# Kernel tuning notes

Hardware: AMD Instinct MI355X
Metric: run time of the kernel (lower is better)

The kernel has to match this reference:

```python
import jax, jax.numpy as jnp
import numpy as np
import math

B, T, N, E = 16, 12, 2000, 8000
D, GAT_HEADS, NHEAD, FF, L, HORIZON = 64, 4, 4, 128, 2, 3
M = B * N  # batched node count


def setup_inputs() -> dict:
    key = jax.random.key(0)
    ks = jax.random.split(key, 16)

    def nrm(k, shape, s=0.1):
        return jax.random.normal(k, shape, jnp.float32) * s

    return dict(
        x_seq=jax.random.normal(ks[0], (B, T, N), jnp.float32),
        edge_index=jax.random.randint(ks[1], (2, E), 0, N),
        # GATConv 1: in_dim=1 -> 4 heads x 8 = 32
        W1=nrm(ks[2], (1, 32)),
        att_src1=nrm(ks[3], (GAT_HEADS, 8)),
        att_dst1=nrm(ks[4], (GAT_HEADS, 8)),
        b1=jnp.zeros((32,), jnp.float32),
        # GATConv 2: 32 -> 4 heads x 16 = 64
        W2=nrm(ks[5], (32, 64)),
        att_src2=nrm(ks[6], (GAT_HEADS, 16)),
        att_dst2=nrm(ks[7], (GAT_HEADS, 16)),
        b2=jnp.zeros((64,), jnp.float32),
        # TransformerEncoder (post-LN, relu), stacked over L layers
        Wqkv=nrm(ks[8], (L, 3 * D, D)), bqkv=jnp.zeros((L, 3 * D), jnp.float32),
        Wo=nrm(ks[9], (L, D, D)), bo=jnp.zeros((L, D), jnp.float32),
        Wf1=nrm(ks[10], (L, FF, D)), bf1=jnp.zeros((L, FF), jnp.float32),
        Wf2=nrm(ks[11], (L, D, FF)), bf2=jnp.zeros((L, D), jnp.float32),
        g1=jnp.ones((L, D), jnp.float32), be1=jnp.zeros((L, D), jnp.float32),
        g2=jnp.ones((L, D), jnp.float32), be2=jnp.zeros((L, D), jnp.float32),
        # prediction head
        Wh=nrm(ks[12], (HORIZON, D)), bh=jnp.zeros((HORIZON,), jnp.float32),
    )


def _layer_norm(x, g, b, eps=1e-5):
    mu = x.mean(-1, keepdims=True)
    var = ((x - mu) ** 2).mean(-1, keepdims=True)
    return (x - mu) * jax.lax.rsqrt(var + eps) * g + b


def _gat(x, src, dst, W, a_src, a_dst, bias, H, C, num_nodes):
    # PyG GATConv (concat=True, eval mode). x: [M, in] -> [M, H*C]
    h = (x @ W).reshape(-1, H, C)                                  # [M,H,C]
    e = jax.nn.leaky_relu((h * a_src).sum(-1)[src] + (h * a_dst).sum(-1)[dst], 0.2)  # [Etot,H]
    m = jax.ops.segment_max(e, dst, num_segments=num_nodes)
    w = jnp.exp(e - m[dst])
    s = jax.ops.segment_sum(w, dst, num_segments=num_nodes)
    alpha = w / (s[dst] + 1e-16)
    out = jax.ops.segment_sum(h[src] * alpha[:, :, None], dst, num_segments=num_nodes)
    return out.reshape(-1, H * C) + bias


def _forward(x_seq, edge_index, W1, att_src1, att_dst1, b1, W2, att_src2, att_dst2, b2,
             Wqkv, bqkv, Wo, bo, Wf1, bf1, Wf2, bf2, g1, be1, g2, be2, Wh, bh):
    # batch edge index with per-graph node offsets, then add self loops (PyG default)
    offs = (jnp.arange(B) * N)[:, None]
    loops = jnp.arange(M)
    src = jnp.concatenate([(edge_index[0][None] + offs).reshape(-1), loops])
    dst = jnp.concatenate([(edge_index[1][None] + offs).reshape(-1), loops])

    xt = x_seq.transpose(1, 0, 2).reshape(T, M, 1)  # per-timestep node features

    def gnn_step(x):
        h = jax.nn.relu(_gat(x, src, dst, W1, att_src1, att_dst1, b1, GAT_HEADS, 8, M))
        return jax.nn.relu(_gat(h, src, dst, W2, att_src2, att_dst2, b2, GAT_HEADS, 16, M))

    seq = jax.vmap(gnn_step)(xt)  # [T, M, D]

    # sinusoidal positional encoding over time axis
    pos = jnp.arange(T, dtype=jnp.float32)[:, None]
    div = jnp.exp(jnp.arange(0, D, 2, dtype=jnp.float32) * (-math.log(10000.0) / D))
    pe = jnp.zeros((T, D), jnp.float32)
    pe = pe.at[:, 0::2].set(jnp.sin(pos * div)).at[:, 1::2].set(jnp.cos(pos * div))
    seq = seq + pe[:, None, :]

    hd = D // NHEAD
    scale = 1.0 / math.sqrt(hd)
    for i in range(L):  # post-LN transformer encoder layers
        qkv = seq @ Wqkv[i].T + bqkv[i]
        q, k, v = jnp.split(qkv, 3, axis=-1)
        q = q.reshape(T, M, NHEAD, hd)
        k = k.reshape(T, M, NHEAD, hd)
        v = v.reshape(T, M, NHEAD, hd)
        sc = jnp.einsum('tmhd,smhd->mhts', q, k) * scale  # [M,H,T,T]
        attn = jax.nn.softmax(sc, axis=-1)
        o = jnp.einsum('mhts,smhd->tmhd', attn, v).reshape(T, M, D)
        seq = _layer_norm(seq + (o @ Wo[i].T + bo[i]), g1[i], be1[i])
        ff = jax.nn.relu(seq @ Wf1[i].T + bf1[i]) @ Wf2[i].T + bf2[i]
        seq = _layer_norm(seq + ff, g2[i], be2[i])

    final = seq[-1]  # [M, D]
    return (final @ Wh.T + bh).reshape(B, N, HORIZON).transpose(0, 2, 1)  # [B, horizon, N]


def reference(x_seq, edge_index, W1, att_src1, att_dst1, b1, W2, att_src2, att_dst2, b2,
              Wqkv, bqkv, Wo, bo, Wf1, bf1, Wf2, bf2, g1, be1, g2, be2, Wh, bh):
    return _forward(x_seq, edge_index, W1, att_src1, att_dst1, b1, W2, att_src2, att_dst2, b2,
                    Wqkv, bqkv, Wo, bo, Wf1, bf1, Wf2, bf2, g1, be1, g2, be2, Wh, bh)
```

## Files before the change

### kernel.cpp

```cpp
#include <hip/hip_runtime.h>
#include <hip/hip_bf16.h>

#define B_ 16
#define T_ 12
#define N_ 2000
#define E_ 8000
#define M_ 32000
#define ETOT (B_*E_ + M_)
#define D_ 64

typedef __hip_bfloat16 bf16;
typedef unsigned short u16;
typedef __attribute__((ext_vector_type(8))) _Float16 half8;
typedef __attribute__((ext_vector_type(2))) _Float16 h2v;
typedef __attribute__((ext_vector_type(4))) float f32x4;

__device__ __forceinline__ float bfu(u16 u){ return __uint_as_float(((unsigned int)u)<<16); }
__device__ __forceinline__ u16 f2bu(float f){
  unsigned int x = __float_as_uint(f);
  x += 0x7FFFu + ((x >> 16) & 1u);
  return (u16)(x >> 16);
}
__device__ __forceinline__ u16 f2h(float f){
  _Float16 h = (_Float16)f; u16 r; __builtin_memcpy(&r, &h, 2); return r;
}
__device__ __forceinline__ float h2f(u16 u){
  _Float16 h; __builtin_memcpy(&h, &u, 2); return (float)h;
}
__device__ __forceinline__ h2v u2h(unsigned u){ h2v r; __builtin_memcpy(&r,&u,4); return r; }

__global__ void k_prep(const float* __restrict__ Wqkv, const float* __restrict__ Wo,
                       const float* __restrict__ Wf1, const float* __restrict__ Wf2,
                       const float* __restrict__ W2g,
                       u16* __restrict__ wqB, u16* __restrict__ woB,
                       u16* __restrict__ w1B, u16* __restrict__ w2B,
                       float* __restrict__ peT, u16* __restrict__ w2gB){
  int i = blockIdx.x*256 + threadIdx.x;
  if(i < 24576){
    int l=i/12288, r=i-l*12288;
    int nt=r>>10, r2=r&1023, c=r2>>9, r3=r2&511, lane=r3>>3, jj=r3&7;
    int m=lane&15, q=lane>>4;
    wqB[i] = f2h(Wqkv[l*12288 + (nt*16+m)*64 + c*32 + q*8 + jj]);
  } else if(i < 32768){
    int k2=i-24576;
    int l=k2>>12, r=k2&4095;
    int nt=r>>10, r2=r&1023, c=r2>>9, r3=r2&511, lane=r3>>3, jj=r3&7;
    int m=lane&15, q=lane>>4;
    woB[k2] = f2h(Wo[l*4096 + (nt*16+m)*64 + c*32 + q*8 + jj]);
  } else if(i < 49152){
    int k2=i-32768;
    int l=k2>>13, r=k2&8191;
    int nt=r>>10, r2=r&1023, c=r2>>9, r3=r2&511, lane=r3>>3, jj=r3&7;
    int m=lane&15, q=lane>>4;
    w1B[k2] = f2h(Wf1[l*8192 + (nt*16+m)*64 + c*32 + q*8 + jj]);
  } else if(i < 65536){
    int k2=i-49152;
    int l=k2>>13, r=k2&8191;
    int nt=r>>11, r2=r&2047, c=r2>>9, r3=r2&511, lane=r3>>3, jj=r3&7;
    int m=lane&15, q=lane>>4;
    w2B[k2] = f2h(Wf2[l*8192 + (nt*16+m)*128 + c*32 + q*8 + jj]);
  } else {
    int i2 = i - 65536;
    if(i2 < 768){
      int t=i2>>6, ch=i2&63;
      float ang = (float)t * __expf(-0.14391156463f * (float)(ch & ~1));
      peT[i2] = (ch&1) ? __cosf(ang) : __sinf(ang);
    } else if(i2 < 768+2048){
      int i3 = i2-768;
      int nt=i3>>9, r=i3&511, lane=r>>3, j=r&7;
      int m=lane&15, q=lane>>4;
      w2gB[i3] = f2h(W2g[(q*8+j)*64 + nt*16 + m]);
    }
  }
}

__global__ void k_hist(const int* __restrict__ ei, int* __restrict__ deg){
  int e = blockIdx.x*256 + threadIdx.x; if(e>=ETOT) return;
  int dst;
  if (e < B_*E_){ int b = e / E_; int k = e - b*E_; dst = ei[E_ + k] + b*N_; }
  else dst = e - B_*E_;
  atomicAdd(&deg[dst], 1);
}

__global__ void k_scan1(const int* __restrict__ deg, int* __restrict__ offs, int* __restrict__ bsums){
  __shared__ int s[256];
  int tid = threadIdx.x; int g = blockIdx.x*256 + tid;
  s[tid] = deg[g]; __syncthreads();
  for(int off=1; off<256; off<<=1){
    int a = (tid>=off) ? s[tid-off] : 0; __syncthreads();
    s[tid] += a; __syncthreads();
  }
  offs[g+1] = s[tid];
  if(tid==255) bsums[blockIdx.x] = s[255];
}

__global__ void k_scan23(int* __restrict__ offs, const int* __restrict__ bsums){
  __shared__ int s[128];
  int tid = threadIdx.x; int g = blockIdx.x*256 + tid;
  if(tid<128) s[tid] = (tid<125) ? bsums[tid] : 0;
  __syncthreads();
  for(int off=1; off<128; off<<=1){
    int a = 0;
    if(tid<128 && tid>=off) a = s[tid-off];
    __syncthreads();
    if(tid<128) s[tid] += a;
    __syncthreads();
  }
  int boff = (blockIdx.x==0) ? 0 : s[blockIdx.x-1];
  offs[g+1] += boff;
  if(g==0) offs[0]=0;
}

__global__ void k_scatter(const int* __restrict__ ei, const int* __restrict__ offs,
                          int* __restrict__ cursor, int* __restrict__ csr){
  int e = blockIdx.x*256 + threadIdx.x; if(e>=ETOT) return;
  int srcl, dst;
  if (e < B_*E_){ int b=e/E_; int k=e-b*E_; srcl=ei[k]; dst=ei[E_+k]+b*N_; }
  else { dst = e - B_*E_; int b=dst/N_; srcl = dst - b*N_; }
  int pos = atomicAdd(&cursor[dst], 1);
  csr[offs[dst]+pos] = srcl;
}

__global__ __launch_bounds__(256) void k_gat12(
  const float* __restrict__ x_seq, const float* __restrict__ W1,
  const float* __restrict__ as1, const float* __restrict__ ad1, const float* __restrict__ b1,
  const float* __restrict__ as2, const float* __restrict__ ad2,
  const int* __restrict__ offs, const int* __restrict__ csr,
  const u16* __restrict__ w2gB,
  u16* __restrict__ h2u, float* __restrict__ asc, float* __restrict__ adc)
{
  int tid = threadIdx.x, w = tid>>6, lane = tid&63;
  int m = lane&15, q = lane>>4;
  int t = blockIdx.y;
  int node = blockIdx.x*64 + w*16 + m;
  unsigned un=(unsigned)node, b=un/N_, n=un-b*N_;

  const half8* wb = (const half8*)w2gB;
  half8 w2f0 = wb[0*64+lane], w2f1 = wb[1*64+lane],
        w2f2 = wb[2*64+lane], w2f3 = wb[3*64+lane];

  float sS[4], sD[4];
  #pragma unroll
  for(int h=0;h<4;h++){
    float a=0.f, d=0.f;
    #pragma unroll
    for(int c=0;c<8;c++){ float wv=W1[h*8+c]; a+=wv*as1[h*8+c]; d+=wv*ad1[h*8+c]; }
    sS[h]=a; sD[h]=d;
  }

  const float* xsl = x_seq + (size_t)(b*T_+t)*N_;
  float xm = xsl[n];
  int e0=offs[node], e1=offs[node+1];
  float sum[4]={0.f,0.f,0.f,0.f}, ax[4]={0.f,0.f,0.f,0.f};
  for(int e=e0+q; e<e1; e+=4){
    float xv = xsl[csr[e]];
    #pragma unroll
    for(int h=0;h<4;h++){
      float ee = xv*sS[h] + xm*sD[h]; ee = ee>0.f ? ee : 0.2f*ee;
      float wv = __expf(ee); sum[h]+=wv; ax[h]+=wv*xv;
    }
  }
  #pragma unroll
  for(int h=0;h<4;h++){
    sum[h] += __shfl_xor(sum[h],16); sum[h] += __shfl_xor(sum[h],32);
    ax[h]  += __shfl_xor(ax[h],16);  ax[h]  += __shfl_xor(ax[h],32);
  }
  float A = ax[q]/(sum[q]+1e-16f);

  half8 af;
  #pragma unroll
  for(int j=0;j<8;j++){
    float v = A*W1[q*8+j] + b1[q*8+j]; v = v>0.f?v:0.f;
    af[j] = (_Float16)v;
  }
  f32x4 ac0={0.f,0.f,0.f,0.f}, ac1=ac0, ac2=ac0, ac3=ac0;
  ac0 = __builtin_amdgcn_mfma_f32_16x16x32_f16(w2f0, af, ac0,0,0,0);
  ac1 = __builtin_amdgcn_mfma_f32_16x16x32_f16(w2f1, af, ac1,0,0,0);
  ac2 = __builtin_amdgcn_mfma_f32_16x16x32_f16(w2f2, af, ac2,0,0,0);
  ac3 = __builtin_amdgcn_mfma_f32_16x16x32_f16(w2f3, af, ac3,0,0,0);

  size_t nd = (size_t)t*M_ + node;
  u16* row = h2u + nd*64;
  {
    uint2 p;
    p.x = (unsigned)f2bu(ac0[0]) | ((unsigned)f2bu(ac0[1])<<16);
    p.y = (unsigned)f2bu(ac0[2]) | ((unsigned)f2bu(ac0[3])<<16);
    *(uint2*)(row + 0*16 + q*4) = p;
    p.x = (unsigned)f2bu(ac1[0]) | ((unsigned)f2bu(ac1[1])<<16);
    p.y = (unsigned)f2bu(ac1[2]) | ((unsigned)f2bu(ac1[3])<<16);
    *(uint2*)(row + 1*16 + q*4) = p;
    p.x = (unsigned)f2bu(ac2[0]) | ((unsigned)f2bu(ac2[1])<<16);
    p.y = (unsigned)f2bu(ac2[2]) | ((unsigned)f2bu(ac2[3])<<16);
    *(uint2*)(row + 2*16 + q*4) = p;
    p.x = (unsigned)f2bu(ac3[0]) | ((unsigned)f2bu(ac3[1])<<16);
    p.y = (unsigned)f2bu(ac3[2]) | ((unsigned)f2bu(ac3[3])<<16);
    *(uint2*)(row + 3*16 + q*4) = p;
  }

  const float* a2sp = as2 + q*4;
  const float* a2dp = ad2 + q*4;
  float ps[4], pd[4];
  ps[0]=ac0[0]*a2sp[ 0]+ac0[1]*a2sp[ 1]+ac0[2]*a2sp[ 2]+ac0[3]*a2sp[ 3];
  ps[1]=ac1[0]*a2sp[16]+ac1[1]*a2sp[17]+ac1[2]*a2sp[18]+ac1[3]*a2sp[19];
  ps[2]=ac2[0]*a2sp[32]+ac2[1]*a2sp[33]+ac2[2]*a2sp[34]+ac2[3]*a2sp[35];
  ps[3]=ac3[0]*a2sp[48]+ac3[1]*a2sp[49]+ac3[2]*a2sp[50]+ac3[3]*a2sp[51];
  pd[0]=ac0[0]*a2dp[ 0]+ac0[1]*a2dp[ 1]+ac0[2]*a2dp[ 2]+ac0[3]*a2dp[ 3];
  pd[1]=ac1[0]*a2dp[16]+ac1[1]*a2dp[17]+ac1[2]*a2dp[18]+ac1[3]*a2dp[19];
  pd[2]=ac2[0]*a2dp[32]+ac2[1]*a2dp[33]+ac2[2]*a2dp[34]+ac2[3]*a2dp[35];
  pd[3]=ac3[0]*a2dp[48]+ac3[1]*a2dp[49]+ac3[2]*a2dp[50]+ac3[3]*a2dp[51];
  #pragma unroll
  for(int h=0;h<4;h++){
    ps[h] += __shfl_xor(ps[h],16); ps[h] += __shfl_xor(ps[h],32);
    pd[h] += __shfl_xor(pd[h],16); pd[h] += __shfl_xor(pd[h],32);
  }
  float ra = (q&1) ? ((q&2)? ps[3]:ps[1]) : ((q&2)? ps[2]:ps[0]);
  float rd = (q&1) ? ((q&2)? pd[3]:pd[1]) : ((q&2)? pd[2]:pd[0]);
  asc[nd*4+q] = ra;
  adc[nd*4+q] = rd;
}

__global__ __launch_bounds__(256) void k_gat2b(
  const u16* __restrict__ h2u, const float* __restrict__ asc, const float* __restrict__ adc,
  const float* __restrict__ b2, const int* __restrict__ offs, const int* __restrict__ csr,
  const float* __restrict__ peT, u16* __restrict__ seq)
{
  int t = blockIdx.y;
  int id = blockIdx.x*256 + threadIdx.x;
  int m = id>>3, j = (id>>2)&1, h = id&3;
  unsigned um=(unsigned)m, b=um/N_;
  size_t base_s = (size_t)t*M_ + (size_t)b*N_;
  float am = adc[((size_t)t*M_+m)*4+h];
  int e0=offs[m], e1=offs[m+1];
  float sum=0.f;
  float A[16];
  #pragma unroll
  for(int c=0;c<16;c++) A[c]=0.f;
  for(int e=e0+j; e<e1; e+=2){
    size_t s = base_s + (unsigned)csr[e];
    float ee = asc[s*4+h] + am; ee = ee>0.f ? ee : 0.2f*ee;
    float w = __expf(ee); sum += w;
    const uint4* hp = (const uint4*)(h2u + s*64 + h*16);
    uint4 p0 = hp[0], p1 = hp[1];
    A[ 0] += w*bfu((u16)(p0.x)); A[ 1] += w*bfu((u16)(p0.x>>16));
    A[ 2] += w*bfu((u16)(p0.y)); A[ 3] += w*bfu((u16)(p0.y>>16));
    A[ 4] += w*bfu((u16)(p0.z)); A[ 5] += w*bfu((u16)(p0.z>>16));
    A[ 6] += w*bfu((u16)(p0.w)); A[ 7] += w*bfu((u16)(p0.w>>16));
    A[ 8] += w*bfu((u16)(p1.x)); A[ 9] += w*bfu((u16)(p1.x>>16));
    A[10] += w*bfu((u16)(p1.y)); A[11] += w*bfu((u16)(p1.y>>16));
    A[12] += w*bfu((u16)(p1.z)); A[13] += w*bfu((u16)(p1.z>>16));
    A[14] += w*bfu((u16)(p1.w)); A[15] += w*bfu((u16)(p1.w>>16));
  }
  sum += __shfl_xor(sum,4);
  #pragma unroll
  for(int c=0;c<16;c++) A[c] += __shfl_xor(A[c],4);

  float inv = 1.f/(sum + 1e-16f);
  u16 ov[8];
  #pragma unroll
  for(int c=0;c<8;c++){
    int ch = h*16 + j*8 + c;
    float v = A[j*8+c]*inv + b2[ch]; v = v>0.f ? v : 0.f;
    ov[c] = f2h(v + peT[t*64+ch]);
  }
  uint4 o;
  o.x = (unsigned)ov[0] | ((unsigned)ov[1]<<16);
  o.y = (unsigned)ov[2] | ((unsigned)ov[3]<<16);
  o.z = (unsigned)ov[4] | ((unsigned)ov[5]<<16);
  o.w = (unsigned)ov[6] | ((unsigned)ov[7]<<16);
  *(uint4*)(seq + ((size_t)t*M_ + m)*64 + h*16 + j*8) = o;
}

__global__ __launch_bounds__(192) void k_layer2(
  const u16* __restrict__ seq,
  const u16* __restrict__ wqB, const u16* __restrict__ woB,
  const u16* __restrict__ w1B, const u16* __restrict__ w2B,
  const float* __restrict__ bqkv, const float* __restrict__ bo,
  const float* __restrict__ bf1,  const float* __restrict__ bf2,
  const float* __restrict__ g1,   const float* __restrict__ be1,
  const float* __restrict__ g2,   const float* __restrict__ be2,
  const float* __restrict__ Wh,   const float* __restrict__ bh,
  float* __restrict__ out)
{
  __shared__ __align__(16) u16 X[3456];
  __shared__ __align__(16) u16 QKV[10368];
  u16* Hd = QKV + 3456;
  int tid=threadIdx.x, w=tid>>6, lane=tid&63;
  int m=lane&15, q=lane>>4;
  int r = w*16 + m;

  #pragma unroll
  for(int half=0; half<2; half++){
    int rr = half*8 + (lane>>3);
    int row = w*16 + rr;
    int nn = row/12, tt = row-nn*12;
    const uint4* src = (const uint4*)(seq + ((size_t)tt*M_ + (size_t)blockIdx.x*4+nn)*64) + (lane&7);
    *((uint4*)&X[row*72] + (lane&7)) = *src;
  }

  #pragma unroll 1
  for(int l=0; l<2; l++){
    const half8* wqv = (const half8*)(wqB + (size_t)l*12288);
    const half8* wov = (const half8*)(woB + (size_t)l*4096);
    const half8* w1v = (const half8*)(w1B + (size_t)l*8192);
    const half8* w2v = (const half8*)(w2B + (size_t)l*8192);
    const float* bq = bqkv + l*192;
    const float* boL = bo + l*64;
    const float* b1L = bf1 + l*128;
    const float* b2L = bf2 + l*64;
    const float* g1L = g1 + l*64, *be1L = be1 + l*64;
    const float* g2L = g2 + l*64, *be2L = be2 + l*64;

    half8 xa0 = *(const half8*)&X[r*72 + q*8];
    half8 xa1 = *(const half8*)&X[r*72 + 32 + q*8];
    #pragma unroll
    for(int nt=0; nt<12; nt++){
      f32x4 acc={0.f,0.f,0.f,0.f};
      acc = __builtin_amdgcn_mfma_f32_16x16x32_f16(xa0, wqv[(nt*2+0)*64+lane], acc,0,0,0);
      acc = __builtin_amdgcn_mfma_f32_16x16x32_f16(xa1, wqv[(nt*2+1)*64+lane], acc,0,0,0);
      int cg = nt*16+m; float bias = bq[cg];
      int s = nt>>2, lc = cg&63;
      #pragma unroll
      for(int rg=0;rg<4;rg++){
        int row = w*16 + q*4 + rg;
        QKV[s*3456 + row*72 + lc] = f2h(acc[rg]+bias);
      }
    }
    __syncthreads();

    {
      int an = tid/48, rem = tid - an*48;
      int ah = rem/12, at = rem - ah*12;
      u16* qrow = &QKV[(an*12+at)*72 + ah*16];
      uint4 qa = ((const uint4*)qrow)[0], qb = ((const uint4*)qrow)[1];
      float s[12];
      #pragma unroll
      for(int t2=0;t2<12;t2++){
        const uint4* kp = (const uint4*)&QKV[3456 + (an*12+t2)*72 + ah*16];
        uint4 ka=kp[0], kb=kp[1];
        float d=0.f;
        d=__builtin_amdgcn_fdot2(u2h(qa.x),u2h(ka.x),d,false);
        d=__builtin_amdgcn_fdot2(u2h(qa.y),u2h(ka.y),d,false);
        d=__builtin_amdgcn_fdot2(u2h(qa.z),u2h(ka.z),d,false);
        d=__builtin_amdgcn_fdot2(u2h(qa.w),u2h(ka.w),d,false);
        d=__builtin_amdgcn_fdot2(u2h(qb.x),u2h(kb.x),d,false);
        d=__builtin_amdgcn_fdot2(u2h(qb.y),u2h(kb.y),d,false);
        d=__builtin_amdgcn_fdot2(u2h(qb.z),u2h(kb.z),d,false);
        d=__builtin_amdgcn_fdot2(u2h(qb.w),u2h(kb.w),d,false);
        s[t2] = d*0.25f;
      }
      float mx=s[0];
      #pragma unroll
      for(int t2=1;t2<12;t2++) mx=fmaxf(mx,s[t2]);
      float sum=0.f;
      #pragma unroll
      for(int t2=0;t2<12;t2++){ s[t2]=__expf(s[t2]-mx); sum+=s[t2]; }
      float inv=1.f/sum;
      half8 o0, o1;
      #pragma unroll
      for(int i=0;i<8;i++){ o0[i]=(_Float16)0.f; o1[i]=(_Float16)0.f; }
      #pragma unroll
      for(int t2=0;t2<12;t2++){
        const half8* vr = (const half8*)&QKV[6912 + (an*12+t2)*72 + ah*16];
        _Float16 wh = (_Float16)s[t2];
        o0 += vr[0]*wh; o1 += vr[1]*wh;
      }
      _Float16 ih = (_Float16)inv;
      ((half8*)qrow)[0]=o0*ih; ((half8*)qrow)[1]=o1*ih;
    }
    __syncthreads();

    half8 oa0 = *(const half8*)&QKV[r*72 + q*8];
    half8 oa1 = *(const half8*)&QKV[r*72 + 32 + q*8];
    float y[4][4];
    #pragma unroll
    for(int nt=0;nt<4;nt++){
      f32x4 acc={0.f,0.f,0.f,0.f};
      acc = __builtin_amdgcn_mfma_f32_16x16x32_f16(oa0, wov[(nt*2+0)*64+lane], acc,0,0,0);
      acc = __builtin_amdgcn_mfma_f32_16x16x32_f16(oa1, wov[(nt*2+1)*64+lane], acc,0,0,0);
      int col=nt*16+m; float bias=boL[col];
      #pragma unroll
      for(int rg=0;rg<4;rg++)
        y[nt][rg] = acc[rg] + bias + h2f(X[(w*16+q*4+rg)*72 + col]);
    }
    float mu[4], rs[4];
    #pragma unroll
    for(int rg=0;rg<4;rg++){
      float sm=(y[0][rg]+y[1][rg])+(y[2][rg]+y[3][rg]);
      sm+=__shfl_xor(sm,1); sm+=__shfl_xor(sm,2); sm+=__shfl_xor(sm,4); sm+=__shfl_xor(sm,8);
      mu[rg]=sm*(1.f/64.f);
      float d0=y[0][rg]-mu[rg],d1=y[1][rg]-mu[rg],d2=y[2][rg]-mu[rg],d3=y[3][rg]-mu[rg];
      float vv=(d0*d0+d1*d1)+(d2*d2+d3*d3);
      vv+=__shfl_xor(vv,1); vv+=__shfl_xor(vv,2); vv+=__shfl_xor(vv,4); vv+=__shfl_xor(vv,8);
      rs[rg]=rsqrtf(vv*(1.f/64.f)+1e-5f);
    }
    #pragma unroll
    for(int nt=0;nt<4;nt++){
      int col=nt*16+m; float g=g1L[col], be=be1L[col];
      #pragma unroll
      for(int rg=0;rg<4;rg++){
        float v=(y[nt][rg]-mu[rg])*rs[rg]*g+be;
        y[nt][rg]=v;
        QKV[(w*16+q*4+rg)*72 + col]=f2h(v);
      }
    }

    half8 ya0 = *(const half8*)&QKV[r*72 + q*8];
    half8 ya1 = *(const half8*)&QKV[r*72 + 32 + q*8];
    #pragma unroll
    for(int nt=0;nt<8;nt++){
      f32x4 acc={0.f,0.f,0.f,0.f};
      acc = __builtin_amdgcn_mfma_f32_16x16x32_f16(ya0, w1v[(nt*2+0)*64+lane], acc,0,0,0);
      acc = __builtin_amdgcn_mfma_f32_16x16x32_f16(ya1, w1v[(nt*2+1)*64+lane], acc,0,0,0);
      float bias=b1L[nt*16+m];
      #pragma unroll
      for(int rg=0;rg<4;rg++)
        Hd[(w*16+q*4+rg)*136 + nt*16+m] = f2h(fmaxf(acc[rg]+bias, 0.f));
    }

    half8 ha[4];
    #pragma unroll
    for(int c=0;c<4;c++)
      ha[c] = *(const half8*)&Hd[r*136 + c*32 + q*8];
    #pragma unroll
    for(int nt=0;nt<4;nt++){
      f32x4 acc={0.f,0.f,0.f,0.f};
      #pragma unroll
      for(int c=0;c<4;c++)
        acc = __builtin_amdgcn_mfma_f32_16x16x32_f16(ha[c], w2v[(nt*4+c)*64+lane], acc,0,0,0);
      int col=nt*16+m; float bias=b2L[col];
      #pragma unroll
      for(int rg=0;rg<4;rg++)
        y[nt][rg] = acc[rg] + bias + y[nt][rg];
    }
    #pragma unroll
    for(int rg=0;rg<4;rg++){
      float sm=(y[0][rg]+y[1][rg])+(y[2][rg]+y[3][rg]);
      sm+=__shfl_xor(sm,1); sm+=__shfl_xor(sm,2); sm+=__shfl_xor(sm,4); sm+=__shfl_xor(sm,8);
      mu[rg]=sm*(1.f/64.f);
      float d0=y[0][rg]-mu[rg],d1=y[1][rg]-mu[rg],d2=y[2][rg]-mu[rg],d3=y[3][rg]-mu[rg];
      float vv=(d0*d0+d1*d1)+(d2*d2+d3*d3);
      vv+=__shfl_xor(vv,1); vv+=__shfl_xor(vv,2); vv+=__shfl_xor(vv,4); vv+=__shfl_xor(vv,8);
      rs[rg]=rsqrtf(vv*(1.f/64.f)+1e-5f);
    }
    if(l==0){
      #pragma unroll
      for(int nt=0;nt<4;nt++){
        int col=nt*16+m; float g=g2L[col], be=be2L[col];
        #pragma unroll
        for(int rg=0;rg<4;rg++)
          X[(w*16+q*4+rg)*72 + col] = f2h((y[nt][rg]-mu[rg])*rs[rg]*g + be);
      }
      __syncthreads();
    } else {
      int rc = w*16 + q*4 + 3;
      int nn = rc/12;
      if(rc - nn*12 == 11){
        float vfin[4];
        #pragma unroll
        for(int nt=0;nt<4;nt++){
          int col=nt*16+m;
          vfin[nt] = (y[nt][3]-mu[3])*rs[3]*g2L[col] + be2L[col];
        }
        int gm = blockIdx.x*4 + nn;
        unsigned bb=(unsigned)gm/N_, n2=(unsigned)gm-bb*N_;
        #pragma unroll
        for(int h3=0;h3<3;h3++){
          float p = vfin[0]*Wh[h3*64+m]    + vfin[1]*Wh[h3*64+16+m]
                  + vfin[2]*Wh[h3*64+32+m] + vfin[3]*Wh[h3*64+48+m];
          p += __shfl_xor(p,1); p += __shfl_xor(p,2);
          p += __shfl_xor(p,4); p += __shfl_xor(p,8);
          if(m==0) out[(bb*3+h3)*N_+n2] = p + bh[h3];
        }
      }
    }
  }
}

extern "C" void kernel_launch(void* const* d_in, const int* in_sizes, int n_in,
                              void* d_out, int out_size, void* d_ws, size_t ws_size,
                              hipStream_t stream)
{
  const float* x_seq=(const float*)d_in[0];
  const int*   ei   =(const int*)d_in[1];
  const float* W1   =(const float*)d_in[2];
  const float* as1  =(const float*)d_in[3];
  const float* ad1  =(const float*)d_in[4];
  const float* b1   =(const float*)d_in[5];
  const float* W2   =(const float*)d_in[6];
  const float* as2  =(const float*)d_in[7];
  const float* ad2  =(const float*)d_in[8];
  const float* b2   =(const float*)d_in[9];
  const float* Wqkv =(const float*)d_in[10];
  const float* bqkv =(const float*)d_in[11];
  const float* Wo   =(const float*)d_in[12];
  const float* bo   =(const float*)d_in[13];
  const float* Wf1  =(const float*)d_in[14];
  const float* bf1p =(const float*)d_in[15];
  const float* Wf2  =(const float*)d_in[16];
  const float* bf2p =(const float*)d_in[17];
  const float* g1   =(const float*)d_in[18];
  const float* be1  =(const float*)d_in[19];
  const float* g2   =(const float*)d_in[20];
  const float* be2  =(const float*)d_in[21];
  const float* Wh   =(const float*)d_in[22];
  const float* bh   =(const float*)d_in[23];

  u16* seqh   = (u16*)d_ws;
  float* asc  = (float*)(seqh + 24576000);
  float* adc  = asc + 1536000;
  int* deg    = (int*)(adc + 1536000);
  int* cursor = deg + M_;
  int* offs   = cursor + M_;
  int* bsums  = offs + (M_ + 2);
  int* boffs  = bsums + 128;
  int* csr    = boffs + 128;
  u16* h2u    = (u16*)(csr + ETOT);
  u16* wqB    = h2u + (size_t)T_*M_*64;
  u16* woB    = wqB + 24576;
  u16* w1B    = woB + 8192;
  u16* w2B    = w1B + 16384;
  float* peT  = (float*)(w2B + 16384);
  u16* w2gB   = (u16*)(peT + 768);

  k_prep   <<<dim3(268), dim3(256), 0, stream>>>(Wqkv, Wo, Wf1, Wf2, W2,
                                                 wqB, woB, w1B, w2B, peT, w2gB);

  hipMemsetAsync(deg, 0, (size_t)2*M_*sizeof(int), stream);
  k_hist   <<<dim3((ETOT+255)/256), dim3(256), 0, stream>>>(ei, deg);
  k_scan1  <<<dim3(125), dim3(256), 0, stream>>>(deg, offs, bsums);
  k_scan23 <<<dim3(125), dim3(256), 0, stream>>>(offs, bsums);
  k_scatter<<<dim3((ETOT+255)/256), dim3(256), 0, stream>>>(ei, offs, cursor, csr);

  k_gat12<<<dim3(500,T_), dim3(256), 0, stream>>>(x_seq, W1, as1, ad1, b1,
                                                  as2, ad2, offs, csr, w2gB,
                                                  h2u, asc, adc);
  k_gat2b<<<dim3(1000,T_), dim3(256), 0, stream>>>(h2u, asc, adc, b2, offs, csr, peT, seqh);

  k_layer2<<<dim3(8000), dim3(192), 0, stream>>>(seqh,
      wqB, woB, w1B, w2B,
      bqkv, bo, bf1p, bf2p,
      g1, be1, g2, be2,
      Wh, bh, (float*)d_out);
}
```

Baseline: 371.4 us.

## Build single-graph CSR and fuse both GAT layers per (batch, timestep) block

Edges are identical across the batch, so the CSR is now built once for the 2000-node graph instead of the batched 32000-node graph. This removes the multi-block scan and shrinks the histogram and scatter work. The two GAT kernels are merged into one 1024-thread kernel per (batch, timestep). It keeps node features and the layer-2 attention logits in shared memory instead of global buffers. The trade-off is a grid of only 192 large blocks, which may leave compute units idle and serialises much of the per-node work inside each block.

```diff
diff --git a/kernel.cpp b/kernel.cpp
--- a/kernel.cpp
+++ b/kernel.cpp
@@ -6,7 +6,7 @@
 #define N_ 2000
 #define E_ 8000
 #define M_ 32000
-#define ETOT (B_*E_ + M_)
+#define EG (E_ + N_)
 #define D_ 64
 
 typedef __hip_bfloat16 bf16;
@@ -74,66 +74,59 @@
   }
 }
 
-__global__ void k_hist(const int* __restrict__ ei, int* __restrict__ deg){
-  int e = blockIdx.x*256 + threadIdx.x; if(e>=ETOT) return;
-  int dst;
-  if (e < B_*E_){ int b = e / E_; int k = e - b*E_; dst = ei[E_ + k] + b*N_; }
-  else dst = e - B_*E_;
+__global__ void k_histg(const int* __restrict__ ei, int* __restrict__ deg){
+  int e = blockIdx.x*256 + threadIdx.x; if(e>=EG) return;
+  int dst = (e < E_) ? ei[E_+e] : e - E_;
   atomicAdd(&deg[dst], 1);
 }
 
-__global__ void k_scan1(const int* __restrict__ deg, int* __restrict__ offs, int* __restrict__ bsums){
-  __shared__ int s[256];
-  int tid = threadIdx.x; int g = blockIdx.x*256 + tid;
-  s[tid] = deg[g]; __syncthreads();
-  for(int off=1; off<256; off<<=1){
-    int a = (tid>=off) ? s[tid-off] : 0; __syncthreads();
-    s[tid] += a; __syncthreads();
-  }
-  offs[g+1] = s[tid];
-  if(tid==255) bsums[blockIdx.x] = s[255];
-}
-
-__global__ void k_scan23(int* __restrict__ offs, const int* __restrict__ bsums){
-  __shared__ int s[128];
-  int tid = threadIdx.x; int g = blockIdx.x*256 + tid;
-  if(tid<128) s[tid] = (tid<125) ? bsums[tid] : 0;
+__global__ __launch_bounds__(1024) void k_scang(const int* __restrict__ deg, int* __restrict__ offs){
+  __shared__ int s[2048];
+  int tid = threadIdx.x;
+  s[tid]      = (tid      < N_) ? deg[tid]      : 0;
+  s[tid+1024] = (tid+1024 < N_) ? deg[tid+1024] : 0;
   __syncthreads();
-  for(int off=1; off<128; off<<=1){
-    int a = 0;
-    if(tid<128 && tid>=off) a = s[tid-off];
+  for(int off=1; off<2048; off<<=1){
+    int a0 = (tid>=off)      ? s[tid-off]      : 0;
+    int a1 = (tid+1024>=off) ? s[tid+1024-off] : 0;
     __syncthreads();
-    if(tid<128) s[tid] += a;
+    s[tid] += a0; s[tid+1024] += a1;
     __syncthreads();
   }
-  int boff = (blockIdx.x==0) ? 0 : s[blockIdx.x-1];
-  offs[g+1] += boff;
-  if(g==0) offs[0]=0;
-}
-
-__global__ void k_scatter(const int* __restrict__ ei, const int* __restrict__ offs,
-                          int* __restrict__ cursor, int* __restrict__ csr){
-  int e = blockIdx.x*256 + threadIdx.x; if(e>=ETOT) return;
+  if(tid      < N_) offs[tid+1]      = s[tid];
+  if(tid+1024 < N_) offs[tid+1024+1] = s[tid+1024];
+  if(tid==0) offs[0]=0;
+}
+
+__global__ void k_scatg(const int* __restrict__ ei, const int* __restrict__ offs,
+                        int* __restrict__ cursor, int* __restrict__ csr){
+  int e = blockIdx.x*256 + threadIdx.x; if(e>=EG) return;
   int srcl, dst;
-  if (e < B_*E_){ int b=e/E_; int k=e-b*E_; srcl=ei[k]; dst=ei[E_+k]+b*N_; }
-  else { dst = e - B_*E_; int b=dst/N_; srcl = dst - b*N_; }
+  if(e < E_){ srcl = ei[e]; dst = ei[E_+e]; }
+  else      { srcl = e - E_; dst = e - E_; }
   int pos = atomicAdd(&cursor[dst], 1);
   csr[offs[dst]+pos] = srcl;
 }
 
-__global__ __launch_bounds__(256) void k_gat12(
+__global__ __launch_bounds__(1024) void k_gat(
   const float* __restrict__ x_seq, const float* __restrict__ W1,
   const float* __restrict__ as1, const float* __restrict__ ad1, const float* __restrict__ b1,
   const float* __restrict__ as2, const float* __restrict__ ad2,
+  const float* __restrict__ b2,  const float* __restrict__ peT,
   const int* __restrict__ offs, const int* __restrict__ csr,
   const u16* __restrict__ w2gB,
-  u16* __restrict__ h2u, float* __restrict__ asc, float* __restrict__ adc)
+  u16* __restrict__ h2u, u16* __restrict__ seq)
 {
-  int tid = threadIdx.x, w = tid>>6, lane = tid&63;
+  __shared__ float xs[N_];
+  __shared__ float ascS[N_*4];
+  __shared__ float adcS[N_*4];
+  int tid = threadIdx.x;
+  int b = blockIdx.x, t = blockIdx.y;
+  const float* xsl = x_seq + (size_t)(b*T_+t)*N_;
+  for(int i=tid;i<N_;i+=1024) xs[i]=xsl[i];
+
+  int wv = tid>>6, lane = tid&63;
   int m = lane&15, q = lane>>4;
-  int t = blockIdx.y;
-  int node = blockIdx.x*64 + w*16 + m;
-  unsigned un=(unsigned)node, b=un/N_, n=un-b*N_;
 
   const half8* wb = (const half8*)w2gB;
   half8 w2f0 = wb[0*64+lane], w2f1 = wb[1*64+lane],
@@ -144,130 +137,127 @@
   for(int h=0;h<4;h++){
     float a=0.f, d=0.f;
     #pragma unroll
-    for(int c=0;c<8;c++){ float wv=W1[h*8+c]; a+=wv*as1[h*8+c]; d+=wv*ad1[h*8+c]; }
+    for(int c=0;c<8;c++){ float w1v=W1[h*8+c]; a+=w1v*as1[h*8+c]; d+=w1v*ad1[h*8+c]; }
     sS[h]=a; sD[h]=d;
   }
-
-  const float* xsl = x_seq + (size_t)(b*T_+t)*N_;
-  float xm = xsl[n];
-  int e0=offs[node], e1=offs[node+1];
-  float sum[4]={0.f,0.f,0.f,0.f}, ax[4]={0.f,0.f,0.f,0.f};
-  for(int e=e0+q; e<e1; e+=4){
-    float xv = xsl[csr[e]];
+  __syncthreads();
+
+  size_t hb = (size_t)t*M_ + (size_t)b*N_;
+
+  for(int chk=wv; chk<125; chk+=16){
+    int nloc = chk*16 + m;
+    float xm = xs[nloc];
+    int e0=offs[nloc], e1=offs[nloc+1];
+    float sum[4]={0.f,0.f,0.f,0.f}, ax[4]={0.f,0.f,0.f,0.f};
+    for(int e=e0+q; e<e1; e+=4){
+      float xv = xs[csr[e]];
+      #pragma unroll
+      for(int h=0;h<4;h++){
+        float ee = xv*sS[h] + xm*sD[h]; ee = ee>0.f ? ee : 0.2f*ee;
+        float wgt = __expf(ee); sum[h]+=wgt; ax[h]+=wgt*xv;
+      }
+    }
     #pragma unroll
     for(int h=0;h<4;h++){
-      float ee = xv*sS[h] + xm*sD[h]; ee = ee>0.f ? ee : 0.2f*ee;
-      float wv = __expf(ee); sum[h]+=wv; ax[h]+=wv*xv;
-    }
-  }
-  #pragma unroll
-  for(int h=0;h<4;h++){
-    sum[h] += __shfl_xor(sum[h],16); sum[h] += __shfl_xor(sum[h],32);
-    ax[h]  += __shfl_xor(ax[h],16);  ax[h]  += __shfl_xor(ax[h],32);
-  }
-  float A = ax[q]/(sum[q]+1e-16f);
-
-  half8 af;
-  #pragma unroll
-  for(int j=0;j<8;j++){
-    float v = A*W1[q*8+j] + b1[q*8+j]; v = v>0.f?v:0.f;
-    af[j] = (_Float16)v;
-  }
-  f32x4 ac0={0.f,0.f,0.f,0.f}, ac1=ac0, ac2=ac0, ac3=ac0;
-  ac0 = __builtin_amdgcn_mfma_f32_16x16x32_f16(w2f0, af, ac0,0,0,0);
-  ac1 = __builtin_amdgcn_mfma_f32_16x16x32_f16(w2f1, af, ac1,0,0,0);
-  ac2 = __builtin_amdgcn_mfma_f32_16x16x32_f16(w2f2, af, ac2,0,0,0);
-  ac3 = __builtin_amdgcn_mfma_f32_16x16x32_f16(w2f3, af, ac3,0,0,0);
-
-  size_t nd = (size_t)t*M_ + node;
-  u16* row = h2u + nd*64;
-  {
-    uint2 p;
-    p.x = (unsigned)f2bu(ac0[0]) | ((unsigned)f2bu(ac0[1])<<16);
-    p.y = (unsigned)f2bu(ac0[2]) | ((unsigned)f2bu(ac0[3])<<16);
-    *(uint2*)(row + 0*16 + q*4) = p;
-    p.x = (unsigned)f2bu(ac1[0]) | ((unsigned)f2bu(ac1[1])<<16);
-    p.y = (unsigned)f2bu(ac1[2]) | ((unsigned)f2bu(ac1[3])<<16);
-    *(uint2*)(row + 1*16 + q*4) = p;
-    p.x = (unsigned)f2bu(ac2[0]) | ((unsigned)f2bu(ac2[1])<<16);
-    p.y = (unsigned)f2bu(ac2[2]) | ((unsigned)f2bu(ac2[3])<<16);
-    *(uint2*)(row + 2*16 + q*4) = p;
-    p.x = (unsigned)f2bu(ac3[0]) | ((unsigned)f2bu(ac3[1])<<16);
-    p.y = (unsigned)f2bu(ac3[2]) | ((unsigned)f2bu(ac3[3])<<16);
-    *(uint2*)(row + 3*16 + q*4) = p;
-  }
-
-  const float* a2sp = as2 + q*4;
-  const float* a2dp = ad2 + q*4;
-  float ps[4], pd[4];
-  ps[0]=ac0[0]*a2sp[ 0]+ac0[1]*a2sp[ 1]+ac0[2]*a2sp[ 2]+ac0[3]*a2sp[ 3];
-  ps[1]=ac1[0]*a2sp[16]+ac1[1]*a2sp[17]+ac1[2]*a2sp[18]+ac1[3]*a2sp[19];
-  ps[2]=ac2[0]*a2sp[32]+ac2[1]*a2sp[33]+ac2[2]*a2sp[34]+ac2[3]*a2sp[35];
-  ps[3]=ac3[0]*a2sp[48]+ac3[1]*a2sp[49]+ac3[2]*a2sp[50]+ac3[3]*a2sp[51];
-  pd[0]=ac0[0]*a2dp[ 0]+ac0[1]*a2dp[ 1]+ac0[2]*a2dp[ 2]+ac0[3]*a2dp[ 3];
-  pd[1]=ac1[0]*a2dp[16]+ac1[1]*a2dp[17]+ac1[2]*a2dp[18]+ac1[3]*a2dp[19];
-  pd[2]=ac2[0]*a2dp[32]+ac2[1]*a2dp[33]+ac2[2]*a2dp[34]+ac2[3]*a2dp[35];
-  pd[3]=ac3[0]*a2dp[48]+ac3[1]*a2dp[49]+ac3[2]*a2dp[50]+ac3[3]*a2dp[51];
-  #pragma unroll
-  for(int h=0;h<4;h++){
-    ps[h] += __shfl_xor(ps[h],16); ps[h] += __shfl_xor(ps[h],32);
-    pd[h] += __shfl_xor(pd[h],16); pd[h] += __shfl_xor(pd[h],32);
-  }
-  float ra = (q&1) ? ((q&2)? ps[3]:ps[1]) : ((q&2)? ps[2]:ps[0]);
-  float rd = (q&1) ? ((q&2)? pd[3]:pd[1]) : ((q&2)? pd[2]:pd[0]);
-  asc[nd*4+q] = ra;
-  adc[nd*4+q] = rd;
-}
-
-__global__ __launch_bounds__(256) void k_gat2b(
-  const u16* __restrict__ h2u, const float* __restrict__ asc, const float* __restrict__ adc,
-  const float* __restrict__ b2, const int* __restrict__ offs, const int* __restrict__ csr,
-  const float* __restrict__ peT, u16* __restrict__ seq)
-{
-  int t = blockIdx.y;
-  int id = blockIdx.x*256 + threadIdx.x;
-  int m = id>>3, j = (id>>2)&1, h = id&3;
-  unsigned um=(unsigned)m, b=um/N_;
-  size_t base_s = (size_t)t*M_ + (size_t)b*N_;
-  float am = adc[((size_t)t*M_+m)*4+h];
-  int e0=offs[m], e1=offs[m+1];
-  float sum=0.f;
-  float A[16];
-  #pragma unroll
-  for(int c=0;c<16;c++) A[c]=0.f;
-  for(int e=e0+j; e<e1; e+=2){
-    size_t s = base_s + (unsigned)csr[e];
-    float ee = asc[s*4+h] + am; ee = ee>0.f ? ee : 0.2f*ee;
-    float w = __expf(ee); sum += w;
-    const uint4* hp = (const uint4*)(h2u + s*64 + h*16);
-    uint4 p0 = hp[0], p1 = hp[1];
-    A[ 0] += w*bfu((u16)(p0.x)); A[ 1] += w*bfu((u16)(p0.x>>16));
-    A[ 2] += w*bfu((u16)(p0.y)); A[ 3] += w*bfu((u16)(p0.y>>16));
-    A[ 4] += w*bfu((u16)(p0.z)); A[ 5] += w*bfu((u16)(p0.z>>16));
-    A[ 6] += w*bfu((u16)(p0.w)); A[ 7] += w*bfu((u16)(p0.w>>16));
-    A[ 8] += w*bfu((u16)(p1.x)); A[ 9] += w*bfu((u16)(p1.x>>16));
-    A[10] += w*bfu((u16)(p1.y)); A[11] += w*bfu((u16)(p1.y>>16));
-    A[12] += w*bfu((u16)(p1.z)); A[13] += w*bfu((u16)(p1.z>>16));
-    A[14] += w*bfu((u16)(p1.w)); A[15] += w*bfu((u16)(p1.w>>16));
-  }
-  sum += __shfl_xor(sum,4);
-  #pragma unroll
-  for(int c=0;c<16;c++) A[c] += __shfl_xor(A[c],4);
-
-  float inv = 1.f/(sum + 1e-16f);
-  u16 ov[8];
-  #pragma unroll
-  for(int c=0;c<8;c++){
-    int ch = h*16 + j*8 + c;
-    float v = A[j*8+c]*inv + b2[ch]; v = v>0.f ? v : 0.f;
-    ov[c] = f2h(v + peT[t*64+ch]);
-  }
-  uint4 o;
-  o.x = (unsigned)ov[0] | ((unsigned)ov[1]<<16);
-  o.y = (unsigned)ov[2] | ((unsigned)ov[3]<<16);
-  o.z = (unsigned)ov[4] | ((unsigned)ov[5]<<16);
-  o.w = (unsigned)ov[6] | ((unsigned)ov[7]<<16);
-  *(uint4*)(seq + ((size_t)t*M_ + m)*64 + h*16 + j*8) = o;
+      sum[h] += __shfl_xor(sum[h],16); sum[h] += __shfl_xor(sum[h],32);
+      ax[h]  += __shfl_xor(ax[h],16);  ax[h]  += __shfl_xor(ax[h],32);
+    }
+    float A = ax[q]/(sum[q]+1e-16f);
+
+    half8 af;
+    #pragma unroll
+    for(int j=0;j<8;j++){
+      float v = A*W1[q*8+j] + b1[q*8+j]; v = v>0.f?v:0.f;
+      af[j] = (_Float16)v;
+    }
+    f32x4 ac0={0.f,0.f,0.f,0.f}, ac1=ac0, ac2=ac0, ac3=ac0;
+    ac0 = __builtin_amdgcn_mfma_f32_16x16x32_f16(w2f0, af, ac0,0,0,0);
+    ac1 = __builtin_amdgcn_mfma_f32_16x16x32_f16(w2f1, af, ac1,0,0,0);
+    ac2 = __builtin_amdgcn_mfma_f32_16x16x32_f16(w2f2, af, ac2,0,0,0);
+    ac3 = __builtin_amdgcn_mfma_f32_16x16x32_f16(w2f3, af, ac3,0,0,0);
+
+    u16* row = h2u + (hb + nloc)*64;
+    {
+      uint2 p;
+      p.x = (unsigned)f2bu(ac0[0]) | ((unsigned)f2bu(ac0[1])<<16);
+      p.y = (unsigned)f2bu(ac0[2]) | ((unsigned)f2bu(ac0[3])<<16);
+      *(uint2*)(row + 0*16 + q*4) = p;
+      p.x = (unsigned)f2bu(ac1[0]) | ((unsigned)f2bu(ac1[1])<<16);
+      p.y = (unsigned)f2bu(ac1[2]) | ((unsigned)f2bu(ac1[3])<<16);
+      *(uint2*)(row + 1*16 + q*4) = p;
+      p.x = (unsigned)f2bu(ac2[0]) | ((unsigned)f2bu(ac2[1])<<16);
+      p.y = (unsigned)f2bu(ac2[2]) | ((unsigned)f2bu(ac2[3])<<16);
+      *(uint2*)(row + 2*16 + q*4) = p;
+      p.x = (unsigned)f2bu(ac3[0]) | ((unsigned)f2bu(ac3[1])<<16);
+      p.y = (unsigned)f2bu(ac3[2]) | ((unsigned)f2bu(ac3[3])<<16);
+      *(uint2*)(row + 3*16 + q*4) = p;
+    }
+
+    const float* a2sp = as2 + q*4;
+    const float* a2dp = ad2 + q*4;
+    float ps[4], pd[4];
+    ps[0]=ac0[0]*a2sp[ 0]+ac0[1]*a2sp[ 1]+ac0[2]*a2sp[ 2]+ac0[3]*a2sp[ 3];
+    ps[1]=ac1[0]*a2sp[16]+ac1[1]*a2sp[17]+ac1[2]*a2sp[18]+ac1[3]*a2sp[19];
+    ps[2]=ac2[0]*a2sp[32]+ac2[1]*a2sp[33]+ac2[2]*a2sp[34]+ac2[3]*a2sp[35];
+    ps[3]=ac3[0]*a2sp[48]+ac3[1]*a2sp[49]+ac3[2]*a2sp[50]+ac3[3]*a2sp[51];
+    pd[0]=ac0[0]*a2dp[ 0]+ac0[1]*a2dp[ 1]+ac0[2]*a2dp[ 2]+ac0[3]*a2dp[ 3];
+    pd[1]=ac1[0]*a2dp[16]+ac1[1]*a2dp[17]+ac1[2]*a2dp[18]+ac1[3]*a2dp[19];
+    pd[2]=ac2[0]*a2dp[32]+ac2[1]*a2dp[33]+ac2[2]*a2dp[34]+ac2[3]*a2dp[35];
+    pd[3]=ac3[0]*a2dp[48]+ac3[1]*a2dp[49]+ac3[2]*a2dp[50]+ac3[3]*a2dp[51];
+    #pragma unroll
+    for(int h=0;h<4;h++){
+      ps[h] += __shfl_xor(ps[h],16); ps[h] += __shfl_xor(ps[h],32);
+      pd[h] += __shfl_xor(pd[h],16); pd[h] += __shfl_xor(pd[h],32);
+    }
+    float ra = (q&1) ? ((q&2)? ps[3]:ps[1]) : ((q&2)? ps[2]:ps[0]);
+    float rd = (q&1) ? ((q&2)? pd[3]:pd[1]) : ((q&2)? pd[2]:pd[0]);
+    ascS[nloc*4+q] = ra;
+    adcS[nloc*4+q] = rd;
+  }
+  __syncthreads();
+
+  for(int id=tid; id<N_*8; id+=1024){
+    int nloc = id>>3, j = (id>>2)&1, h = id&3;
+    float am = adcS[nloc*4+h];
+    int e0=offs[nloc], e1=offs[nloc+1];
+    float sum=0.f;
+    float A[16];
+    #pragma unroll
+    for(int c=0;c<16;c++) A[c]=0.f;
+    for(int e=e0+j; e<e1; e+=2){
+      int s = csr[e];
+      float ee = ascS[s*4+h] + am; ee = ee>0.f ? ee : 0.2f*ee;
+      float wgt = __expf(ee); sum += wgt;
+      const uint4* hp = (const uint4*)(h2u + (hb + s)*64 + h*16);
+      uint4 p0 = hp[0], p1 = hp[1];
+      A[ 0] += wgt*bfu((u16)(p0.x)); A[ 1] += wgt*bfu((u16)(p0.x>>16));
+      A[ 2] += wgt*bfu((u16)(p0.y)); A[ 3] += wgt*bfu((u16)(p0.y>>16));
+      A[ 4] += wgt*bfu((u16)(p0.z)); A[ 5] += wgt*bfu((u16)(p0.z>>16));
+      A[ 6] += wgt*bfu((u16)(p0.w)); A[ 7] += wgt*bfu((u16)(p0.w>>16));
+      A[ 8] += wgt*bfu((u16)(p1.x)); A[ 9] += wgt*bfu((u16)(p1.x>>16));
+      A[10] += wgt*bfu((u16)(p1.y)); A[11] += wgt*bfu((u16)(p1.y>>16));
+      A[12] += wgt*bfu((u16)(p1.z)); A[13] += wgt*bfu((u16)(p1.z>>16));
+      A[14] += wgt*bfu((u16)(p1.w)); A[15] += wgt*bfu((u16)(p1.w>>16));
+    }
+    sum += __shfl_xor(sum,4);
+    #pragma unroll
+    for(int c=0;c<16;c++) A[c] += __shfl_xor(A[c],4);
+
+    float inv = 1.f/(sum + 1e-16f);
+    u16 ov[8];
+    #pragma unroll
+    for(int c=0;c<8;c++){
+      int chn = h*16 + j*8 + c;
+      float v = A[j*8+c]*inv + b2[chn]; v = v>0.f ? v : 0.f;
+      ov[c] = f2h(v + peT[t*64+chn]);
+    }
+    uint4 o;
+    o.x = (unsigned)ov[0] | ((unsigned)ov[1]<<16);
+    o.y = (unsigned)ov[2] | ((unsigned)ov[3]<<16);
+    o.z = (unsigned)ov[4] | ((unsigned)ov[5]<<16);
+    o.w = (unsigned)ov[6] | ((unsigned)ov[7]<<16);
+    *(uint4*)(seq + (hb + nloc)*64 + h*16 + j*8) = o;
+  }
 }
 
 __global__ __launch_bounds__(192) void k_layer2(
@@ -506,35 +496,30 @@
   const float* bh   =(const float*)d_in[23];
 
   u16* seqh   = (u16*)d_ws;
-  float* asc  = (float*)(seqh + 24576000);
-  float* adc  = asc + 1536000;
-  int* deg    = (int*)(adc + 1536000);
-  int* cursor = deg + M_;
-  int* offs   = cursor + M_;
-  int* bsums  = offs + (M_ + 2);
-  int* boffs  = bsums + 128;
-  int* csr    = boffs + 128;
-  u16* h2u    = (u16*)(csr + ETOT);
-  u16* wqB    = h2u + (size_t)T_*M_*64;
+  u16* h2u    = seqh + 24576000;
+  u16* wqB    = h2u + 24576000;
   u16* woB    = wqB + 24576;
   u16* w1B    = woB + 8192;
   u16* w2B    = w1B + 16384;
   float* peT  = (float*)(w2B + 16384);
   u16* w2gB   = (u16*)(peT + 768);
+  int* deg    = (int*)(w2gB + 2048);
+  int* cursor = deg + N_;
+  int* offs   = cursor + N_;
+  int* csr    = offs + (N_ + 2);
 
   k_prep   <<<dim3(268), dim3(256), 0, stream>>>(Wqkv, Wo, Wf1, Wf2, W2,
                                                  wqB, woB, w1B, w2B, peT, w2gB);
 
-  hipMemsetAsync(deg, 0, (size_t)2*M_*sizeof(int), stream);
-  k_hist   <<<dim3((ETOT+255)/256), dim3(256), 0, stream>>>(ei, deg);
-  k_scan1  <<<dim3(125), dim3(256), 0, stream>>>(deg, offs, bsums);
-  k_scan23 <<<dim3(125), dim3(256), 0, stream>>>(offs, bsums);
-  k_scatter<<<dim3((ETOT+255)/256), dim3(256), 0, stream>>>(ei, offs, cursor, csr);
-
-  k_gat12<<<dim3(500,T_), dim3(256), 0, stream>>>(x_seq, W1, as1, ad1, b1,
-                                                  as2, ad2, offs, csr, w2gB,
-                                                  h2u, asc, adc);
-  k_gat2b<<<dim3(1000,T_), dim3(256), 0, stream>>>(h2u, asc, adc, b2, offs, csr, peT, seqh);
+  hipMemsetAsync(deg, 0, (size_t)2*N_*sizeof(int), stream);
+  k_histg <<<dim3((EG+255)/256), dim3(256), 0, stream>>>(ei, deg);
+  k_scang <<<dim3(1), dim3(1024), 0, stream>>>(deg, offs);
+  k_scatg <<<dim3((EG+255)/256), dim3(256), 0, stream>>>(ei, offs, cursor, csr);
+
+  k_gat<<<dim3(B_, T_), dim3(1024), 0, stream>>>(x_seq, W1, as1, ad1, b1,
+                                                 as2, ad2, b2, peT,
+                                                 offs, csr, w2gB,
+                                                 h2u, seqh);
 
   k_layer2<<<dim3(8000), dim3(192), 0, stream>>>(seqh,
       wqB, woB, w1B, w2B,
```

New measurement: 365.1 us. No clear change (-1.7%).
